# Kernel optimization log

Hardware: AMD Instinct MI355X
Metric: run time of the kernel (lower is better)

Reference implementation:

```python
import jax, jax.numpy as jnp
import numpy as np

B, C_IN, T = 8, 1024, 4096
VQ_C, CODEBOOK, DS = 1024, 2048, 2


def setup_inputs() -> dict:
    key = jax.random.key(0)
    ks = jax.random.split(key, 6)
    return {
        "x": jax.random.normal(ks[0], (B, C_IN, T), jnp.float32),
        "x_mask": jnp.ones((B, 1, T), jnp.float32),
        "w_in": jax.random.normal(ks[1], (VQ_C, C_IN, DS), jnp.float32) * 0.02,
        "b_in": jnp.zeros((VQ_C,), jnp.float32),
        "embed": jax.random.normal(ks[2], (CODEBOOK, VQ_C), jnp.float32),
        "w_out": jax.random.normal(ks[3], (C_IN, VQ_C), jnp.float32) * 0.02,
        "b_out": jnp.zeros((C_IN,), jnp.float32),
    }


def reference(x, x_mask, w_in, b_in, embed, w_out, b_out):
    x_len = x.shape[2]
    ds = w_in.shape[-1]
    pad = (-x_len) % ds  # static under jit
    if pad:
        x = jnp.pad(x, ((0, 0), (0, 0), (0, pad)))
        x_mask = jnp.pad(x_mask, ((0, 0), (0, 0), (0, pad)))
    b, cin, tp = x.shape
    # conv_in: Conv1d(k=ds, stride=ds) == non-overlapping window contraction
    h = jnp.einsum('bcls,ocs->bol', x.reshape(b, cin, tp // ds, ds), w_in) + b_in[None, :, None]  # [B, D, L]
    tokens = h.transpose(0, 2, 1)  # [B, L, D]
    # euclidean codebook: ||t - e||^2 expanded (stable for argmin)
    d2 = (jnp.sum(tokens * tokens, -1, keepdims=True)
          - 2.0 * jnp.einsum('bld,nd->bln', tokens, embed)
          + jnp.sum(embed * embed, -1)[None, None, :])  # [B, L, N]
    idx = jnp.argmin(d2, axis=-1)  # [B, L]
    q = embed[idx]  # gather -> [B, L, D]
    # commitment loss (training-mode math; EMA codebook -> embed not a grad path)
    commit_loss = jnp.mean((jax.lax.stop_gradient(q) - tokens) ** 2)
    # straight-through estimator
    q_st = tokens + jax.lax.stop_gradient(q - tokens)
    q_cf = q_st.transpose(0, 2, 1)  # [B, D, L]
    # conv_out: nearest upsample x ds, then 1x1 conv
    up = jnp.repeat(q_cf, ds, axis=2)  # [B, D, Tp]
    out = jnp.einsum('bct,oc->bot', up, w_out) + b_out[None, :, None]
    out = out * x_mask
    return out[:, :, :x_len], commit_loss
```

## Files before the change

kernel.cpp:

```cpp
#include <hip/hip_runtime.h>

typedef _Float16 half8 __attribute__((ext_vector_type(8)));
typedef float f32x4 __attribute__((ext_vector_type(4)));

static constexpr int D = 1024;
static constexpr int NCODE = 2048;
static constexpr int MTOK = 16384;
static constexpr int KIN = 2048;
static constexpr int TLEN = 4096;
static constexpr int CAP = 2048;
#define TAU 0.4f

__device__ __forceinline__ void gload16(const void* g, void* l) {
  __builtin_amdgcn_global_load_lds(
      (const __attribute__((address_space(1))) void*)g,
      (__attribute__((address_space(3))) void*)l, 16, 0, 0);
}

#define SBAR()   asm volatile("s_barrier" ::: "memory")
#define WAITV4() asm volatile("s_waitcnt vmcnt(4)" ::: "memory")
#define WAITV0() asm volatile("s_waitcnt vmcnt(0)" ::: "memory")

__device__ __forceinline__ float key_to_f32(unsigned u) {
  unsigned bits = (u & 0x80000000u) ? (u & 0x7FFFFFFFu) : ~u;
  return __uint_as_float(bits);
}
__device__ __forceinline__ unsigned f32_to_key(float f) {
  unsigned ub = __float_as_uint(f);
  return (ub & 0x80000000u) ? ~ub : (ub | 0x80000000u);
}

__global__ __launch_bounds__(256) void k_pack_x(const float* __restrict__ x,
                                                _Float16* __restrict__ xh,
                                                _Float16* __restrict__ xl) {
  __shared__ float lds[32][65];
  const int tt0 = blockIdx.x * 64;
  const int cc0 = blockIdx.y * 32;
  const int b = blockIdx.z;
  const float* xb = x + ((size_t)b * D + cc0) * TLEN + tt0;
#pragma unroll
  for (int i = 0; i < 8; ++i) {
    int idx = threadIdx.x + i * 256;
    lds[idx >> 6][idx & 63] = xb[(size_t)(idx >> 6) * TLEN + (idx & 63)];
  }
  __syncthreads();
  const size_t mrow0 = (size_t)b * 2048 + (tt0 >> 1);
  const int r = threadIdx.x >> 3;
  const int g = threadIdx.x & 7;
  half8 vh, vl;
#pragma unroll
  for (int j = 0; j < 8; ++j) {
    int kk = g * 8 + j;
    float v = lds[kk >> 1][2 * r + (kk & 1)];
    _Float16 h = (_Float16)v;
    vh[j] = h;
    vl[j] = (_Float16)(v - (float)h);
  }
  size_t off = (mrow0 + r) * (size_t)KIN + (size_t)cc0 * 2 + g * 8;
  *(half8*)(xh + off) = vh;
  *(half8*)(xl + off) = vl;
}

__global__ __launch_bounds__(256) void k_split(const float* __restrict__ s,
                                               _Float16* __restrict__ hi,
                                               _Float16* __restrict__ lo, int n) {
  int i = blockIdx.x * 256 + threadIdx.x;
  if (i < n) {
    float v = s[i];
    _Float16 h = (_Float16)v;
    hi[i] = h;
    lo[i] = (_Float16)(v - (float)h);
  }
}

__global__ __launch_bounds__(256) void k_e2(const float* __restrict__ embed,
                                            float* __restrict__ e2c) {
  int row = blockIdx.x * 4 + (threadIdx.x >> 6);
  int lane = threadIdx.x & 63;
  const float* er = embed + (size_t)row * D;
  double s = 0.0;
  for (int i = lane; i < D; i += 64) { double v = er[i]; s += v * v; }
#pragma unroll
  for (int mk = 1; mk < 64; mk <<= 1) s += __shfl_xor(s, mk, 64);
  if (lane == 0) e2c[row] = (float)(s - 1024.0);
}

template <int KDIM, int LOG_GX, int MODE>
__global__ __launch_bounds__(512, 2) void k_gemm_hh(
    const _Float16* __restrict__ Ah_, const _Float16* __restrict__ Bh_,
    const float* __restrict__ vec,
    _Float16* __restrict__ outh, float* __restrict__ t2,
    unsigned long long* __restrict__ skKey, float* __restrict__ skSnd) {
  __shared__ _Float16 lds[3 * 16384];
  const int nwg = gridDim.x, bid = blockIdx.x, q = nwg >> 3;
  const int b2 = (bid & 7) * q + (bid >> 3);
  const int nb = b2 & ((1 << LOG_GX) - 1);
  const int n0 = nb * 256, m0 = (b2 >> LOG_GX) * 256;
  const int tid = threadIdx.x, lane = tid & 63, w = tid >> 6;
  const int wr = w >> 2, wc = w & 3, lr = lane & 15, lk = lane >> 4;
  constexpr int NT = KDIM / 32;
  const int cswz8 = (((lane & 3) ^ ((lane >> 3) & 3))) * 8;
  const int rswz8 = (lk ^ ((lr >> 1) & 3)) * 8;

  f32x4 acc[8][4] = {};

  auto stage = [&](int t, int c) {
    char* sb = (char*)(lds + c * 16384);
    const int k0 = t * 32;
    const int r0 = (w * 64 + lane) >> 2;
    gload16(Ah_ + (size_t)(m0 + r0) * KDIM + k0 + cswz8, sb + w * 1024);
    gload16(Ah_ + (size_t)(m0 + 128 + r0) * KDIM + k0 + cswz8, sb + w * 1024 + 8192);
    gload16(Bh_ + (size_t)(n0 + r0) * KDIM + k0 + cswz8, sb + 16384 + w * 1024);
    gload16(Bh_ + (size_t)(n0 + 128 + r0) * KDIM + k0 + cswz8, sb + 16384 + w * 1024 + 8192);
  };

  stage(0, 0);
  stage(1, 1);
  WAITV4();
  SBAR();

  int c0 = 0, c1 = 1, c2 = 2;
  for (int t = 0; t < NT; ++t) {
    const bool st = (t + 2) < NT;
    if (st) stage(t + 2, c2);
    const _Float16* sb = lds + c0 * 16384;
    half8 ah[8], bh[4];
#pragma unroll
    for (int f = 0; f < 8; ++f)
      ah[f] = *(const half8*)(sb + (wr * 128 + f * 16 + lr) * 32 + rswz8);
#pragma unroll
    for (int f = 0; f < 4; ++f)
      bh[f] = *(const half8*)(sb + 8192 + (wc * 64 + f * 16 + lr) * 32 + rswz8);
    __builtin_amdgcn_s_setprio(1);
#pragma unroll
    for (int fm = 0; fm < 8; ++fm)
#pragma unroll
      for (int fn = 0; fn < 4; ++fn)
        acc[fm][fn] = __builtin_amdgcn_mfma_f32_16x16x32_f16(ah[fm], bh[fn], acc[fm][fn], 0, 0, 0);
    __builtin_amdgcn_s_setprio(0);
    if (st) { WAITV4(); } else if (t + 1 < NT) { WAITV0(); }
    SBAR();
    int tmp = c0; c0 = c1; c1 = c2; c2 = tmp;
  }

  if constexpr (MODE == 0) {
#pragma unroll
    for (int fm = 0; fm < 8; ++fm) {
#pragma unroll
      for (int j = 0; j < 4; ++j) {
        int row = wr * 128 + fm * 16 + lk * 4 + j;
        size_t m = (size_t)m0 + row;
        float v2 = 0.f;
#pragma unroll
        for (int fn = 0; fn < 4; ++fn) {
          int col = n0 + wc * 64 + fn * 16 + lr;
          float v = acc[fm][fn][j] + vec[col];
          v2 += v * v;
          outh[m * (size_t)D + col] = (_Float16)v;
        }
#pragma unroll
        for (int mk = 1; mk < 16; mk <<= 1) v2 += __shfl_xor(v2, mk, 64);
        if (lr == 0) atomicAdd(&t2[m], v2);
      }
    }
  } else {
#pragma unroll
    for (int fm = 0; fm < 8; ++fm) {
#pragma unroll
      for (int j = 0; j < 4; ++j) {
        int row = wr * 128 + fm * 16 + lk * 4 + j;
        size_t m = (size_t)m0 + row;
        float b1 = 3.4e38f, bb2 = 3.4e38f;
        int i1 = 0x7FFFFFFF;
#pragma unroll
        for (int fn = 0; fn < 4; ++fn) {
          int col = n0 + wc * 64 + fn * 16 + lr;
          float mv = vec[col] - 2.0f * acc[fm][fn][j];
          if (mv < b1) { bb2 = b1; b1 = mv; i1 = col; }
          else if (mv < bb2) { bb2 = mv; }
        }
#pragma unroll
        for (int mk = 1; mk < 16; mk <<= 1) {
          float ob1 = __shfl_xor(b1, mk, 64);
          float ob2 = __shfl_xor(bb2, mk, 64);
          int oi = __shfl_xor(i1, mk, 64);
          if (ob1 < b1) { bb2 = fminf(b1, ob2); b1 = ob1; i1 = oi; }
          else { bb2 = fminf(bb2, ob1); }
        }
        if (lr == 0) {
          unsigned long long key = ((unsigned long long)f32_to_key(b1) << 32) | (unsigned)i1;
          skKey[m * 32 + nb * 4 + wc] = key;
          skSnd[m * 32 + nb * 4 + wc] = bb2;
        }
      }
    }
  }
}

__global__ __launch_bounds__(256) void k_flag(const unsigned long long* __restrict__ skKey,
                                              const float* __restrict__ skSnd,
                                              unsigned long long* __restrict__ keys,
                                              int* __restrict__ list, int* __restrict__ counter) {
  int m = blockIdx.x * 256 + threadIdx.x;
  unsigned long long best = ~0ull;
  int bsl = 0;
#pragma unroll
  for (int sl = 0; sl < 32; ++sl) {
    unsigned long long k = skKey[(size_t)m * 32 + sl];
    if (k < best) { best = k; bsl = sl; }
  }
  float b1 = key_to_f32((unsigned)(best >> 32));
  float second = skSnd[(size_t)m * 32 + bsl];
#pragma unroll
  for (int sl = 0; sl < 32; ++sl) {
    if (sl != bsl) second = fminf(second, key_to_f32((unsigned)(skKey[(size_t)m * 32 + sl] >> 32)));
  }
  keys[m] = best;
  if (second - b1 < TAU) {
    int p = atomicAdd(counter, 1);
    if (p < CAP) list[p] = m;
  }
}

__global__ __launch_bounds__(256) void k_tok_fix(
    const _Float16* __restrict__ xh, const _Float16* __restrict__ xl,
    const _Float16* __restrict__ wh, const _Float16* __restrict__ wl,
    const float* __restrict__ b_in, const int* __restrict__ list,
    const int* __restrict__ counter,
    _Float16* __restrict__ tokh2, _Float16* __restrict__ tokl2) {
  const int count = min(counter[0], CAP);
  const int m0 = blockIdx.y * 128;
  if (m0 >= count) return;
  __shared__ _Float16 sAh[128 * 32], sAl[128 * 32], sBh[128 * 32], sBl[128 * 32];
  const int n0 = blockIdx.x * 128;
  const int tid = threadIdx.x, lane = tid & 63, w = tid >> 6;
  const int wr = w >> 1, wc = w & 1, lr = lane & 15, lk = lane >> 4;
  f32x4 acc[4][4] = {};

  const int g0 = w * 128 + lane, g1 = g0 + 64;
  const int rA0 = g0 >> 2, cA0 = g0 & 3, rA1 = g1 >> 2, cA1 = g1 & 3;
  const int lb0 = (w * 128) * 16, lb1 = (w * 128 + 64) * 16;
  const int tk0 = list[min(m0 + rA0, count - 1)];
  const int tk1 = list[min(m0 + rA1, count - 1)];

  for (int kt = 0; kt < KIN / 32; ++kt) {
    const int k0 = kt * 32;
    gload16(xh + (size_t)tk0 * KIN + k0 + cA0 * 8, (char*)sAh + lb0);
    gload16(xh + (size_t)tk1 * KIN + k0 + cA1 * 8, (char*)sAh + lb1);
    gload16(xl + (size_t)tk0 * KIN + k0 + cA0 * 8, (char*)sAl + lb0);
    gload16(xl + (size_t)tk1 * KIN + k0 + cA1 * 8, (char*)sAl + lb1);
    gload16(wh + (size_t)(n0 + rA0) * KIN + k0 + cA0 * 8, (char*)sBh + lb0);
    gload16(wh + (size_t)(n0 + rA1) * KIN + k0 + cA1 * 8, (char*)sBh + lb1);
    gload16(wl + (size_t)(n0 + rA0) * KIN + k0 + cA0 * 8, (char*)sBl + lb0);
    gload16(wl + (size_t)(n0 + rA1) * KIN + k0 + cA1 * 8, (char*)sBl + lb1);
    __syncthreads();
    half8 ah[4], al2[4], bh[4], bl2[4];
#pragma unroll
    for (int f = 0; f < 4; ++f) {
      ah[f]  = *(const half8*)(sAh + (wr * 64 + f * 16 + lr) * 32 + lk * 8);
      al2[f] = *(const half8*)(sAl + (wr * 64 + f * 16 + lr) * 32 + lk * 8);
      bh[f]  = *(const half8*)(sBh + (wc * 64 + f * 16 + lr) * 32 + lk * 8);
      bl2[f] = *(const half8*)(sBl + (wc * 64 + f * 16 + lr) * 32 + lk * 8);
    }
#pragma unroll
    for (int fm = 0; fm < 4; ++fm)
#pragma unroll
      for (int fn = 0; fn < 4; ++fn) {
        acc[fm][fn] = __builtin_amdgcn_mfma_f32_16x16x32_f16(ah[fm], bh[fn], acc[fm][fn], 0, 0, 0);
        acc[fm][fn] = __builtin_amdgcn_mfma_f32_16x16x32_f16(ah[fm], bl2[fn], acc[fm][fn], 0, 0, 0);
        acc[fm][fn] = __builtin_amdgcn_mfma_f32_16x16x32_f16(al2[fm], bh[fn], acc[fm][fn], 0, 0, 0);
      }
    __syncthreads();
  }
#pragma unroll
  for (int fm = 0; fm < 4; ++fm) {
#pragma unroll
    for (int j = 0; j < 4; ++j) {
      int row = wr * 64 + fm * 16 + lk * 4 + j;
      if (m0 + row >= count) continue;
#pragma unroll
      for (int fn = 0; fn < 4; ++fn) {
        int col = n0 + wc * 64 + fn * 16 + lr;
        float v = acc[fm][fn][j] + b_in[col];
        _Float16 h = (_Float16)v;
        tokh2[(size_t)(m0 + row) * D + col] = h;
        tokl2[(size_t)(m0 + row) * D + col] = (_Float16)(v - (float)h);
      }
    }
  }
}

__global__ __launch_bounds__(256) void k_rescore(
    const _Float16* __restrict__ tokh2, const _Float16* __restrict__ tokl2,
    const _Float16* __restrict__ eh, const _Float16* __restrict__ el,
    const float* __restrict__ e2c, const int* __restrict__ list,
    const int* __restrict__ counter,
    unsigned long long* __restrict__ keys2) {
  const int count = min(counter[0], CAP);
  const int m0 = blockIdx.y * 128;
  if (m0 >= count) return;
  __shared__ _Float16 sAh[128 * 32], sAl[128 * 32], sBh[128 * 32], sBl[128 * 32];
  const int n0 = blockIdx.x * 128;
  const int tid = threadIdx.x, lane = tid & 63, w = tid >> 6;
  const int wr = w >> 1, wc = w & 1, lr = lane & 15, lk = lane >> 4;
  f32x4 acc[4][4] = {};

  const int g0 = w * 128 + lane, g1 = g0 + 64;
  const int rA0 = g0 >> 2, cA0 = g0 & 3, rA1 = g1 >> 2, cA1 = g1 & 3;
  const int lb0 = (w * 128) * 16, lb1 = (w * 128 + 64) * 16;

  for (int kt = 0; kt < D / 32; ++kt) {
    const int k0 = kt * 32;
    gload16(tokh2 + (size_t)(m0 + rA0) * D + k0 + cA0 * 8, (char*)sAh + lb0);
    gload16(tokh2 + (size_t)(m0 + rA1) * D + k0 + cA1 * 8, (char*)sAh + lb1);
    gload16(tokl2 + (size_t)(m0 + rA0) * D + k0 + cA0 * 8, (char*)sAl + lb0);
    gload16(tokl2 + (size_t)(m0 + rA1) * D + k0 + cA1 * 8, (char*)sAl + lb1);
    gload16(eh + (size_t)(n0 + rA0) * D + k0 + cA0 * 8, (char*)sBh + lb0);
    gload16(eh + (size_t)(n0 + rA1) * D + k0 + cA1 * 8, (char*)sBh + lb1);
    gload16(el + (size_t)(n0 + rA0) * D + k0 + cA0 * 8, (char*)sBl + lb0);
    gload16(el + (size_t)(n0 + rA1) * D + k0 + cA1 * 8, (char*)sBl + lb1);
    __syncthreads();
    half8 ah[4], al2[4], bh[4], bl2[4];
#pragma unroll
    for (int f = 0; f < 4; ++f) {
      ah[f]  = *(const half8*)(sAh + (wr * 64 + f * 16 + lr) * 32 + lk * 8);
      al2[f] = *(const half8*)(sAl + (wr * 64 + f * 16 + lr) * 32 + lk * 8);
      bh[f]  = *(const half8*)(sBh + (wc * 64 + f * 16 + lr) * 32 + lk * 8);
      bl2[f] = *(const half8*)(sBl + (wc * 64 + f * 16 + lr) * 32 + lk * 8);
    }
#pragma unroll
    for (int fm = 0; fm < 4; ++fm)
#pragma unroll
      for (int fn = 0; fn < 4; ++fn) {
        acc[fm][fn] = __builtin_amdgcn_mfma_f32_16x16x32_f16(ah[fm], bh[fn], acc[fm][fn], 0, 0, 0);
        acc[fm][fn] = __builtin_amdgcn_mfma_f32_16x16x32_f16(ah[fm], bl2[fn], acc[fm][fn], 0, 0, 0);
        acc[fm][fn] = __builtin_amdgcn_mfma_f32_16x16x32_f16(al2[fm], bh[fn], acc[fm][fn], 0, 0, 0);
      }
    __syncthreads();
  }
#pragma unroll
  for (int fm = 0; fm < 4; ++fm) {
#pragma unroll
    for (int j = 0; j < 4; ++j) {
      int row = wr * 64 + fm * 16 + lk * 4 + j;
      if (m0 + row >= count) continue;
      int tm = list[m0 + row];
      float best = 3.4e38f;
      int bidx = 0x7FFFFFFF;
#pragma unroll
      for (int fn = 0; fn < 4; ++fn) {
        int col = n0 + wc * 64 + fn * 16 + lr;
        float mv = e2c[col] - 2.0f * acc[fm][fn][j];
        if (mv < best) { best = mv; bidx = col; }
      }
#pragma unroll
      for (int mk = 1; mk < 16; mk <<= 1) {
        float ob = __shfl_xor(best, mk, 64);
        int oi = __shfl_xor(bidx, mk, 64);
        if (ob < best || (ob == best && oi < bidx)) { best = ob; bidx = oi; }
      }
      if (lr == 0) {
        unsigned long long key = ((unsigned long long)f32_to_key(best) << 32) | (unsigned)bidx;
        atomicMin(&keys2[tm], key);
      }
    }
  }
}

__global__ __launch_bounds__(256) void k_merge(unsigned long long* __restrict__ keys,
                                               const unsigned long long* __restrict__ keys2) {
  int m = blockIdx.x * 256 + threadIdx.x;
  unsigned long long k2 = keys2[m];
  if (k2 != ~0ull) keys[m] = k2;
}

__global__ __launch_bounds__(256) void k_F(
    const _Float16* __restrict__ eh, const _Float16* __restrict__ el,
    const _Float16* __restrict__ woh, const _Float16* __restrict__ wol,
    const float* __restrict__ b_out, float* __restrict__ F) {
  __shared__ _Float16 sAh[128 * 32], sAl[128 * 32], sBh[128 * 32], sBl[128 * 32];
  const int n0 = blockIdx.x * 128, m0 = blockIdx.y * 128;
  const int tid = threadIdx.x, lane = tid & 63, w = tid >> 6;
  const int wr = w >> 1, wc = w & 1, lr = lane & 15, lk = lane >> 4;
  f32x4 acc[4][4] = {};

  const int g0 = w * 128 + lane, g1 = g0 + 64;
  const int rA0 = g0 >> 2, cA0 = g0 & 3, rA1 = g1 >> 2, cA1 = g1 & 3;
  const int lb0 = (w * 128) * 16, lb1 = (w * 128 + 64) * 16;

  for (int kt = 0; kt < D / 32; ++kt) {
    const int k0 = kt * 32;
    gload16(eh + (size_t)(m0 + rA0) * D + k0 + cA0 * 8, (char*)sAh + lb0);
    gload16(eh + (size_t)(m0 + rA1) * D + k0 + cA1 * 8, (char*)sAh + lb1);
    gload16(el + (size_t)(m0 + rA0) * D + k0 + cA0 * 8, (char*)sAl + lb0);
    gload16(el + (size_t)(m0 + rA1) * D + k0 + cA1 * 8, (char*)sAl + lb1);
    gload16(woh + (size_t)(n0 + rA0) * D + k0 + cA0 * 8, (char*)sBh + lb0);
    gload16(woh + (size_t)(n0 + rA1) * D + k0 + cA1 * 8, (char*)sBh + lb1);
    gload16(wol + (size_t)(n0 + rA0) * D + k0 + cA0 * 8, (char*)sBl + lb0);
    gload16(wol + (size_t)(n0 + rA1) * D + k0 + cA1 * 8, (char*)sBl + lb1);
    __syncthreads();
    half8 ah[4], al2[4], bh[4], bl2[4];
#pragma unroll
    for (int f = 0; f < 4; ++f) {
      ah[f]  = *(const half8*)(sAh + (wr * 64 + f * 16 + lr) * 32 + lk * 8);
      al2[f] = *(const half8*)(sAl + (wr * 64 + f * 16 + lr) * 32 + lk * 8);
      bh[f]  = *(const half8*)(sBh + (wc * 64 + f * 16 + lr) * 32 + lk * 8);
      bl2[f] = *(const half8*)(sBl + (wc * 64 + f * 16 + lr) * 32 + lk * 8);
    }
#pragma unroll
    for (int fm = 0; fm < 4; ++fm)
#pragma unroll
      for (int fn = 0; fn < 4; ++fn) {
        acc[fm][fn] = __builtin_amdgcn_mfma_f32_16x16x32_f16(ah[fm], bh[fn], acc[fm][fn], 0, 0, 0);
        acc[fm][fn] = __builtin_amdgcn_mfma_f32_16x16x32_f16(ah[fm], bl2[fn], acc[fm][fn], 0, 0, 0);
        acc[fm][fn] = __builtin_amdgcn_mfma_f32_16x16x32_f16(al2[fm], bh[fn], acc[fm][fn], 0, 0, 0);
      }
    __syncthreads();
  }
#pragma unroll
  for (int fm = 0; fm < 4; ++fm)
#pragma unroll
    for (int j = 0; j < 4; ++j) {
      int row = wr * 64 + fm * 16 + lk * 4 + j;
#pragma unroll
      for (int fn = 0; fn < 4; ++fn) {
        int col = n0 + wc * 64 + fn * 16 + lr;
        F[(size_t)(m0 + row) * D + col] = acc[fm][fn][j] + b_out[col];
      }
    }
}

__global__ __launch_bounds__(256) void k_expand(
    const float* __restrict__ F, const unsigned long long* __restrict__ keys,
    const float* __restrict__ mask, float* __restrict__ out) {
  __shared__ float ldsF[64 * 67];
  const int b = blockIdx.y;
  const int t0 = blockIdx.x * 128;
  const int ocbase = blockIdx.z * 512;
  const int tid = threadIdx.x;

  const int tok_w = tid & 63, ocr = tid >> 6;
  const float2 mv = *(const float2*)&mask[(size_t)b * TLEN + t0 + 2 * tok_w];
  float* outb = out + ((size_t)b * D) * TLEN + t0 + 2 * tok_w;

  const int ltk = tid >> 2, lg = tid & 3;
  const unsigned lidx = (unsigned)(keys[b * 2048 + (t0 >> 1) + ltk] & 0xFFFFFFFFull);
  const float* Fl = F + (size_t)lidx * D + lg * 16;

  for (int c8 = 0; c8 < 8; ++c8) {
    const int oc0 = ocbase + c8 * 64;
#pragma unroll
    for (int j = 0; j < 16; ++j)
      ldsF[ltk * 67 + lg * 16 + j] = Fl[oc0 + j];
    __syncthreads();
#pragma unroll
    for (int i = 0; i < 16; ++i) {
      int c = ocr + i * 4;
      float v = ldsF[tok_w * 67 + c];
      float2 o; o.x = v * mv.x; o.y = v * mv.y;
      *(float2*)&outb[(size_t)(oc0 + c) * TLEN] = o;
    }
    __syncthreads();
  }
}

__global__ __launch_bounds__(256) void k_loss(const unsigned long long* __restrict__ keys,
                                              const float* __restrict__ t2,
                                              double* __restrict__ acc) {
  int m = blockIdx.x * 256 + threadIdx.x;
  unsigned long long k = keys[m];
  float mval = key_to_f32((unsigned)(k >> 32));
  double c = (double)mval + 1024.0 + (double)t2[m];
#pragma unroll
  for (int mk = 1; mk < 64; mk <<= 1) c += __shfl_xor(c, mk, 64);
  __shared__ double part[4];
  if ((threadIdx.x & 63) == 0) part[threadIdx.x >> 6] = c;
  __syncthreads();
  if (threadIdx.x == 0) atomicAdd(acc, part[0] + part[1] + part[2] + part[3]);
}

__global__ void k_finalize(const double* __restrict__ acc, float* __restrict__ dst) {
  if (threadIdx.x == 0 && blockIdx.x == 0) *dst = (float)(*acc * (1.0 / 16777216.0));
}

extern "C" void kernel_launch(void* const* d_in, const int* in_sizes, int n_in,
                              void* d_out, int out_size, void* d_ws, size_t ws_size,
                              hipStream_t stream) {
  (void)in_sizes; (void)n_in; (void)out_size;
  const float* x      = (const float*)d_in[0];
  const float* xmask  = (const float*)d_in[1];
  const float* w_in   = (const float*)d_in[2];
  const float* b_in   = (const float*)d_in[3];
  const float* embed  = (const float*)d_in[4];
  const float* w_out  = (const float*)d_in[5];
  const float* b_out  = (const float*)d_in[6];
  float* out = (float*)d_out;

  _Float16* xh = (_Float16*)d_out;
  _Float16* xl = xh + (size_t)MTOK * KIN;

  char* p = (char*)d_ws;
  auto take = [&](size_t sz) { char* r = p; p += (sz + 255) & ~(size_t)255; return r; };
  _Float16* wh    = (_Float16*)take((size_t)D * KIN * 2);
  _Float16* wl    = (_Float16*)take((size_t)D * KIN * 2);
  _Float16* eh    = (_Float16*)take((size_t)NCODE * D * 2);
  _Float16* el    = (_Float16*)take((size_t)NCODE * D * 2);
  _Float16* woh   = (_Float16*)take((size_t)D * D * 2);
  _Float16* wol   = (_Float16*)take((size_t)D * D * 2);
  float* Fm       = (float*)take((size_t)NCODE * D * 4);
  float* e2c      = (float*)take((size_t)NCODE * 4);
  _Float16* tokh  = (_Float16*)take((size_t)MTOK * D * 2);
  _Float16* tokh2 = (_Float16*)take((size_t)CAP * D * 2);
  _Float16* tokl2 = (_Float16*)take((size_t)CAP * D * 2);
  float* t2       = (float*)take((size_t)MTOK * 4);
  unsigned long long* keys  = (unsigned long long*)take((size_t)MTOK * 8);
  unsigned long long* keys2 = (unsigned long long*)take((size_t)MTOK * 8);
  unsigned long long* skKey = (unsigned long long*)take((size_t)MTOK * 32 * 8);
  float* skSnd    = (float*)take((size_t)MTOK * 32 * 4);
  int* list       = (int*)take((size_t)CAP * 4);
  int* counter    = (int*)take(256);
  double* lossacc = (double*)take(256);
  if ((size_t)(p - (char*)d_ws) > ws_size) return;

  hipMemsetAsync(keys2, 0xFF, (size_t)MTOK * 8, stream);
  hipMemsetAsync(t2, 0, (size_t)MTOK * 4, stream);
  hipMemsetAsync(list, 0, (size_t)CAP * 4, stream);
  hipMemsetAsync(counter, 0, 256, stream);
  hipMemsetAsync(lossacc, 0, 8, stream);

  k_pack_x<<<dim3(64, 32, 8), 256, 0, stream>>>(x, xh, xl);
  k_split<<<(D * KIN + 255) / 256, 256, 0, stream>>>(w_in, wh, wl, D * KIN);
  k_split<<<(NCODE * D + 255) / 256, 256, 0, stream>>>(embed, eh, el, NCODE * D);
  k_split<<<(D * D + 255) / 256, 256, 0, stream>>>(w_out, woh, wol, D * D);
  k_e2<<<NCODE / 4, 256, 0, stream>>>(embed, e2c);

  k_F<<<dim3(D / 128, NCODE / 128), 256, 0, stream>>>(eh, el, woh, wol, b_out, Fm);

  k_gemm_hh<KIN, 2, 0><<<256, 512, 0, stream>>>(xh, wh, b_in, tokh, t2, nullptr, nullptr);
  k_gemm_hh<D, 3, 1><<<512, 512, 0, stream>>>(tokh, eh, e2c, nullptr, nullptr, skKey, skSnd);
  k_flag<<<MTOK / 256, 256, 0, stream>>>(skKey, skSnd, keys, list, counter);
  k_tok_fix<<<dim3(D / 128, CAP / 128), 256, 0, stream>>>(xh, xl, wh, wl, b_in, list, counter, tokh2, tokl2);
  k_rescore<<<dim3(NCODE / 128, CAP / 128), 256, 0, stream>>>(tokh2, tokl2, eh, el, e2c, list, counter, keys2);
  k_merge<<<MTOK / 256, 256, 0, stream>>>(keys, keys2);

  k_expand<<<dim3(TLEN / 128, 8, 2), 256, 0, stream>>>(Fm, keys, xmask, out);

  k_loss<<<MTOK / 256, 256, 0, stream>>>(keys, t2, lossacc);
  k_finalize<<<1, 64, 0, stream>>>(lossacc, out + (size_t)MTOK * KIN);
}
```

Baseline: 457.8 us.

## Retile GEMMs to 1024-thread blocks and drop memsets, merge and atomic pass

The two main fp16 GEMMs are re-parameterised with a BM template. They now run with 1024-thread workgroups, one per CU, sharing a single 256-wide B tile across more waves, with wait counts adjusted to match. The per-token squared norm is no longer accumulated atomically in the first GEMM epilogue. A separate k_t2 kernel computes it from the fp16 tokens, which slightly changes the precision of the loss term. The separate memsets and the k_merge kernel are removed: counter and loss resets move into k_e2, keys2 is reset in k_flag, and consumers pick keys2 over keys inline.

Result: slower. 931.3 us (+103.5%).

```diff
diff --git a/kernel.cpp b/kernel.cpp
--- a/kernel.cpp
+++ b/kernel.cpp
@@ -18,7 +18,8 @@
 }
 
 #define SBAR()   asm volatile("s_barrier" ::: "memory")
-#define WAITV4() asm volatile("s_waitcnt vmcnt(4)" ::: "memory")
+#define WAITV3() asm volatile("s_waitcnt vmcnt(3)" ::: "memory")
+#define WAITV2() asm volatile("s_waitcnt vmcnt(2)" ::: "memory")
 #define WAITV0() asm volatile("s_waitcnt vmcnt(0)" ::: "memory")
 
 __device__ __forceinline__ float key_to_f32(unsigned u) {
@@ -74,7 +75,10 @@
 }
 
 __global__ __launch_bounds__(256) void k_e2(const float* __restrict__ embed,
-                                            float* __restrict__ e2c) {
+                                            float* __restrict__ e2c,
+                                            int* __restrict__ counter,
+                                            double* __restrict__ lossacc) {
+  if (blockIdx.x == 0 && threadIdx.x == 0) { counter[0] = 0; lossacc[0] = 0.0; }
   int row = blockIdx.x * 4 + (threadIdx.x >> 6);
   int lane = threadIdx.x & 63;
   const float* er = embed + (size_t)row * D;
@@ -85,90 +89,89 @@
   if (lane == 0) e2c[row] = (float)(s - 1024.0);
 }
 
-template <int KDIM, int LOG_GX, int MODE>
-__global__ __launch_bounds__(512, 2) void k_gemm_hh(
+template <int KDIM, int BM, int LOG_GX, int MODE>
+__global__ __launch_bounds__(1024, 1) void k_gemm_hh(
     const _Float16* __restrict__ Ah_, const _Float16* __restrict__ Bh_,
     const float* __restrict__ vec,
-    _Float16* __restrict__ outh, float* __restrict__ t2,
+    _Float16* __restrict__ outh,
     unsigned long long* __restrict__ skKey, float* __restrict__ skSnd) {
-  __shared__ _Float16 lds[3 * 16384];
+  constexpr int M_REP = BM / 64;
+  constexpr int AH = BM * 32;
+  constexpr int BUF = AH + 8192;
+  constexpr int NT = KDIM / 32;
+  __shared__ _Float16 lds[3 * BUF];
+
   const int nwg = gridDim.x, bid = blockIdx.x, q = nwg >> 3;
   const int b2 = (bid & 7) * q + (bid >> 3);
   const int nb = b2 & ((1 << LOG_GX) - 1);
-  const int n0 = nb * 256, m0 = (b2 >> LOG_GX) * 256;
+  const int n0 = nb * 256, m0 = (b2 >> LOG_GX) * BM;
   const int tid = threadIdx.x, lane = tid & 63, w = tid >> 6;
   const int wr = w >> 2, wc = w & 3, lr = lane & 15, lk = lane >> 4;
-  constexpr int NT = KDIM / 32;
   const int cswz8 = (((lane & 3) ^ ((lane >> 3) & 3))) * 8;
   const int rswz8 = (lk ^ ((lr >> 1) & 3)) * 8;
 
-  f32x4 acc[8][4] = {};
+  f32x4 acc[M_REP][4] = {};
 
   auto stage = [&](int t, int c) {
-    char* sb = (char*)(lds + c * 16384);
+    char* sb = (char*)(lds + c * BUF);
     const int k0 = t * 32;
-    const int r0 = (w * 64 + lane) >> 2;
-    gload16(Ah_ + (size_t)(m0 + r0) * KDIM + k0 + cswz8, sb + w * 1024);
-    gload16(Ah_ + (size_t)(m0 + 128 + r0) * KDIM + k0 + cswz8, sb + w * 1024 + 8192);
-    gload16(Bh_ + (size_t)(n0 + r0) * KDIM + k0 + cswz8, sb + 16384 + w * 1024);
-    gload16(Bh_ + (size_t)(n0 + 128 + r0) * KDIM + k0 + cswz8, sb + 16384 + w * 1024 + 8192);
+    const int row = tid >> 2;
+    gload16(Ah_ + (size_t)(m0 + row) * KDIM + k0 + cswz8, sb + w * 1024);
+    if constexpr (BM == 512)
+      gload16(Ah_ + (size_t)(m0 + 256 + row) * KDIM + k0 + cswz8, sb + 16384 + w * 1024);
+    gload16(Bh_ + (size_t)(n0 + row) * KDIM + k0 + cswz8, sb + AH * 2 + w * 1024);
   };
+  auto waitc = [&]() { if constexpr (BM == 512) WAITV3(); else WAITV2(); };
 
   stage(0, 0);
   stage(1, 1);
-  WAITV4();
+  waitc();
   SBAR();
 
   int c0 = 0, c1 = 1, c2 = 2;
   for (int t = 0; t < NT; ++t) {
     const bool st = (t + 2) < NT;
     if (st) stage(t + 2, c2);
-    const _Float16* sb = lds + c0 * 16384;
-    half8 ah[8], bh[4];
-#pragma unroll
-    for (int f = 0; f < 8; ++f)
-      ah[f] = *(const half8*)(sb + (wr * 128 + f * 16 + lr) * 32 + rswz8);
+    const _Float16* sb = lds + c0 * BUF;
+    half8 ah[M_REP], bh[4];
+#pragma unroll
+    for (int f = 0; f < M_REP; ++f)
+      ah[f] = *(const half8*)(sb + (wr * (BM / 4) + f * 16 + lr) * 32 + rswz8);
 #pragma unroll
     for (int f = 0; f < 4; ++f)
-      bh[f] = *(const half8*)(sb + 8192 + (wc * 64 + f * 16 + lr) * 32 + rswz8);
+      bh[f] = *(const half8*)(sb + AH + (wc * 64 + f * 16 + lr) * 32 + rswz8);
     __builtin_amdgcn_s_setprio(1);
 #pragma unroll
-    for (int fm = 0; fm < 8; ++fm)
+    for (int fm = 0; fm < M_REP; ++fm)
 #pragma unroll
       for (int fn = 0; fn < 4; ++fn)
         acc[fm][fn] = __builtin_amdgcn_mfma_f32_16x16x32_f16(ah[fm], bh[fn], acc[fm][fn], 0, 0, 0);
     __builtin_amdgcn_s_setprio(0);
-    if (st) { WAITV4(); } else if (t + 1 < NT) { WAITV0(); }
+    if (st) { waitc(); } else if (t + 1 < NT) { WAITV0(); }
     SBAR();
     int tmp = c0; c0 = c1; c1 = c2; c2 = tmp;
   }
 
   if constexpr (MODE == 0) {
 #pragma unroll
-    for (int fm = 0; fm < 8; ++fm) {
+    for (int fm = 0; fm < M_REP; ++fm) {
 #pragma unroll
       for (int j = 0; j < 4; ++j) {
-        int row = wr * 128 + fm * 16 + lk * 4 + j;
+        int row = wr * (BM / 4) + fm * 16 + lk * 4 + j;
         size_t m = (size_t)m0 + row;
-        float v2 = 0.f;
 #pragma unroll
         for (int fn = 0; fn < 4; ++fn) {
           int col = n0 + wc * 64 + fn * 16 + lr;
-          float v = acc[fm][fn][j] + vec[col];
-          v2 += v * v;
-          outh[m * (size_t)D + col] = (_Float16)v;
+          outh[m * (size_t)D + col] = (_Float16)(acc[fm][fn][j] + vec[col]);
         }
-#pragma unroll
-        for (int mk = 1; mk < 16; mk <<= 1) v2 += __shfl_xor(v2, mk, 64);
-        if (lr == 0) atomicAdd(&t2[m], v2);
       }
     }
   } else {
 #pragma unroll
-    for (int fm = 0; fm < 8; ++fm) {
+    for (int fm = 0; fm < M_REP; ++fm) {
 #pragma unroll
       for (int j = 0; j < 4; ++j) {
-        int row = wr * 128 + fm * 16 + lk * 4 + j;
+        int row = wr * (BM / 4) + fm * 16 + lk * 4 + j;
         size_t m = (size_t)m0 + row;
         float b1 = 3.4e38f, bb2 = 3.4e38f;
         int i1 = 0x7FFFFFFF;
@@ -197,11 +200,30 @@
   }
 }
 
+__global__ __launch_bounds__(256) void k_t2(const _Float16* __restrict__ tokh,
+                                            float* __restrict__ t2) {
+  const int w = threadIdx.x >> 6, lane = threadIdx.x & 63;
+  const int row = blockIdx.x * 4 + w;
+  const _Float16* tr = tokh + (size_t)row * D + lane * 16;
+  float s = 0.f;
+#pragma unroll
+  for (int v = 0; v < 2; ++v) {
+    half8 h = *(const half8*)(tr + v * 8);
+#pragma unroll
+    for (int j = 0; j < 8; ++j) { float f = (float)h[j]; s += f * f; }
+  }
+#pragma unroll
+  for (int mk = 1; mk < 64; mk <<= 1) s += __shfl_xor(s, mk, 64);
+  if (lane == 0) t2[row] = s;
+}
+
 __global__ __launch_bounds__(256) void k_flag(const unsigned long long* __restrict__ skKey,
                                               const float* __restrict__ skSnd,
                                               unsigned long long* __restrict__ keys,
+                                              unsigned long long* __restrict__ keys2,
                                               int* __restrict__ list, int* __restrict__ counter) {
   int m = blockIdx.x * 256 + threadIdx.x;
+  keys2[m] = ~0ull;
   unsigned long long best = ~0ull;
   int bsl = 0;
 #pragma unroll
@@ -367,13 +389,6 @@
   }
 }
 
-__global__ __launch_bounds__(256) void k_merge(unsigned long long* __restrict__ keys,
-                                               const unsigned long long* __restrict__ keys2) {
-  int m = blockIdx.x * 256 + threadIdx.x;
-  unsigned long long k2 = keys2[m];
-  if (k2 != ~0ull) keys[m] = k2;
-}
-
 __global__ __launch_bounds__(256) void k_F(
     const _Float16* __restrict__ eh, const _Float16* __restrict__ el,
     const _Float16* __restrict__ woh, const _Float16* __restrict__ wol,
@@ -432,6 +447,7 @@
 
 __global__ __launch_bounds__(256) void k_expand(
     const float* __restrict__ F, const unsigned long long* __restrict__ keys,
+    const unsigned long long* __restrict__ keys2,
     const float* __restrict__ mask, float* __restrict__ out) {
   __shared__ float ldsF[64 * 67];
   const int b = blockIdx.y;
@@ -444,7 +460,10 @@
   float* outb = out + ((size_t)b * D) * TLEN + t0 + 2 * tok_w;
 
   const int ltk = tid >> 2, lg = tid & 3;
-  const unsigned lidx = (unsigned)(keys[b * 2048 + (t0 >> 1) + ltk] & 0xFFFFFFFFull);
+  const int lm = b * 2048 + (t0 >> 1) + ltk;
+  unsigned long long kk = keys2[lm];
+  if (kk == ~0ull) kk = keys[lm];
+  const unsigned lidx = (unsigned)(kk & 0xFFFFFFFFull);
   const float* Fl = F + (size_t)lidx * D + lg * 16;
 
   for (int c8 = 0; c8 < 8; ++c8) {
@@ -465,10 +484,12 @@
 }
 
 __global__ __launch_bounds__(256) void k_loss(const unsigned long long* __restrict__ keys,
+                                              const unsigned long long* __restrict__ keys2,
                                               const float* __restrict__ t2,
                                               double* __restrict__ acc) {
   int m = blockIdx.x * 256 + threadIdx.x;
-  unsigned long long k = keys[m];
+  unsigned long long k = keys2[m];
+  if (k == ~0ull) k = keys[m];
   float mval = key_to_f32((unsigned)(k >> 32));
   double c = (double)mval + 1024.0 + (double)t2[m];
 #pragma unroll
@@ -522,29 +543,23 @@
   double* lossacc = (double*)take(256);
   if ((size_t)(p - (char*)d_ws) > ws_size) return;
 
-  hipMemsetAsync(keys2, 0xFF, (size_t)MTOK * 8, stream);
-  hipMemsetAsync(t2, 0, (size_t)MTOK * 4, stream);
-  hipMemsetAsync(list, 0, (size_t)CAP * 4, stream);
-  hipMemsetAsync(counter, 0, 256, stream);
-  hipMemsetAsync(lossacc, 0, 8, stream);
-
   k_pack_x<<<dim3(64, 32, 8), 256, 0, stream>>>(x, xh, xl);
   k_split<<<(D * KIN + 255) / 256, 256, 0, stream>>>(w_in, wh, wl, D * KIN);
   k_split<<<(NCODE * D + 255) / 256, 256, 0, stream>>>(embed, eh, el, NCODE * D);
   k_split<<<(D * D + 255) / 256, 256, 0, stream>>>(w_out, woh, wol, D * D);
-  k_e2<<<NCODE / 4, 256, 0, stream>>>(embed, e2c);
+  k_e2<<<NCODE / 4, 256, 0, stream>>>(embed, e2c, counter, lossacc);
 
   k_F<<<dim3(D / 128, NCODE / 128), 256, 0, stream>>>(eh, el, woh, wol, b_out, Fm);
 
-  k_gemm_hh<KIN, 2, 0><<<256, 512, 0, stream>>>(xh, wh, b_in, tokh, t2, nullptr, nullptr);
-  k_gemm_hh<D, 3, 1><<<512, 512, 0, stream>>>(tokh, eh, e2c, nullptr, nullptr, skKey, skSnd);
-  k_flag<<<MTOK / 256, 256, 0, stream>>>(skKey, skSnd, keys, list, counter);
+  k_gemm_hh<KIN, 256, 2, 0><<<256, 1024, 0, stream>>>(xh, wh, b_in, tokh, nullptr, nullptr);
+  k_t2<<<MTOK / 4, 256, 0, stream>>>(tokh, t2);
+  k_gemm_hh<D, 512, 3, 1><<<256, 1024, 0, stream>>>(tokh, eh, e2c, nullptr, skKey, skSnd);
+  k_flag<<<MTOK / 256, 256, 0, stream>>>(skKey, skSnd, keys, keys2, list, counter);
   k_tok_fix<<<dim3(D / 128, CAP / 128), 256, 0, stream>>>(xh, xl, wh, wl, b_in, list, counter, tokh2, tokl2);
   k_rescore<<<dim3(NCODE / 128, CAP / 128), 256, 0, stream>>>(tokh2, tokl2, eh, el, e2c, list, counter, keys2);
-  k_merge<<<MTOK / 256, 256, 0, stream>>>(keys, keys2);
-
-  k_expand<<<dim3(TLEN / 128, 8, 2), 256, 0, stream>>>(Fm, keys, xmask, out);
-
-  k_loss<<<MTOK / 256, 256, 0, stream>>>(keys, t2, lossacc);
+
+  k_expand<<<dim3(TLEN / 128, 8, 2), 256, 0, stream>>>(Fm, keys, keys2, xmask, out);
+
+  k_loss<<<MTOK / 256, 256, 0, stream>>>(keys, keys2, t2, lossacc);
   k_finalize<<<1, 64, 0, stream>>>(lossacc, out + (size_t)MTOK * KIN);
 }
```
